# Performance work log

Measured on AMD Instinct MI355X. Metric: run time of the kernel, lower is better.

The kernel has to match this reference:

```python
import jax, jax.numpy as jnp
import numpy as np

IN_DIM = 128
D_MODEL = 2 * IN_DIM        # 256, Mamba d_model
D_INNER = 2 * D_MODEL       # 512, expand=2
D_STATE = 16
D_CONV = 4
DT_RANK = (D_MODEL + 15) // 16  # 16
B = 4
C = 1024                    # original channel dim -> Mamba sequence length
EPS = 1e-5


def rmsnorm(x, w):
    return x * jax.lax.rsqrt(jnp.mean(x * x, axis=-1, keepdims=True) + EPS) * w


def conv1x1(x, w, b):
    # x: (B, Cin, L); 1x1 conv == channel matmul
    return jnp.einsum('oi,bil->bol', w, x) + b[None, :, None]


def mamba(u, in_w, conv_w, conv_b, xproj_w, dt_w, dt_b, A_log, Dp, out_w):
    # u: (B, L, D_MODEL) -- faithful mamba_ssm Mamba block (defaults)
    di, K = conv_w.shape
    n = A_log.shape[1]
    r = dt_w.shape[1]
    xz = u @ in_w.T                              # (B,L,2*di)
    xx, z = jnp.split(xz, 2, axis=-1)
    # depthwise causal conv over L
    xt = jnp.pad(jnp.transpose(xx, (0, 2, 1)), ((0, 0), (0, 0), (K - 1, 0)))
    xc = jax.lax.conv_general_dilated(xt, conv_w[:, None, :], (1,), 'VALID',
                                      feature_group_count=di)
    xx = jax.nn.silu(jnp.transpose(xc + conv_b[None, :, None], (0, 2, 1)))
    dbl = xx @ xproj_w.T                         # (B,L,r+2n)
    dt, Bm, Cm = dbl[..., :r], dbl[..., r:r + n], dbl[..., r + n:]
    dt = jax.nn.softplus(dt @ dt_w.T + dt_b)     # (B,L,di)
    A = -jnp.exp(A_log)                          # (di,n)
    dA = jnp.exp(dt[..., None] * A)              # (B,L,di,n)
    dBx = (dt * xx)[..., None] * Bm[:, :, None, :]

    def step(h, inps):
        dA_t, dBx_t, C_t = inps
        h = dA_t * h + dBx_t
        return h, jnp.einsum('bdn,bn->bd', h, C_t)

    h0 = jnp.zeros((u.shape[0], di, n), u.dtype)
    _, ys = jax.lax.scan(step, h0, (jnp.moveaxis(dA, 1, 0),
                                    jnp.moveaxis(dBx, 1, 0),
                                    jnp.moveaxis(Cm, 1, 0)))
    y = jnp.moveaxis(ys, 0, 1) + xx * Dp
    return (y * jax.nn.silu(z)) @ out_w.T


def postnorm_mamba(u, params, norm_w):
    return rmsnorm(mamba(u, *params), norm_w) + u


def _forward(x, W_in, b_in, W_wp, b_wp, W_fp, b_fp, W_bp, b_bp, W_out, b_out,
             norm_w_top,
             f_in_w, f_conv_w, f_conv_b, f_xproj_w, f_dt_w, f_dt_b, f_A_log, f_D, f_out_w, f_norm_w,
             bk_in_w, bk_conv_w, bk_conv_b, bk_xproj_w, bk_dt_w, bk_dt_b, bk_A_log, bk_D, bk_out_w, bk_norm_w):
    residual = x                                  # (B, C, L)
    xn = rmsnorm(x, norm_w_top)                   # RMSNorm over L
    xt = jnp.transpose(xn, (0, 2, 1))             # (B, L, C); L acts as conv channels
    ssm_in = conv1x1(xt, W_in, b_in)              # (B, 2L, C)
    # forward branch
    fwd = conv1x1(ssm_in, W_fp, b_fp)
    fwd = jnp.transpose(fwd, (0, 2, 1))           # (B, C, 2L): Mamba seq=C
    fwd = postnorm_mamba(fwd, (f_in_w, f_conv_w, f_conv_b, f_xproj_w, f_dt_w,
                               f_dt_b, f_A_log, f_D, f_out_w), f_norm_w)
    fwd = jnp.transpose(fwd, (0, 2, 1))           # (B, 2L, C)
    # backward branch (flip along C)
    bwd = conv1x1(ssm_in[:, :, ::-1], W_bp, b_bp)
    bwd = jnp.transpose(bwd, (0, 2, 1))
    bwd = postnorm_mamba(bwd, (bk_in_w, bk_conv_w, bk_conv_b, bk_xproj_w, bk_dt_w,
                               bk_dt_b, bk_A_log, bk_D, bk_out_w), bk_norm_w)
    bwd = jnp.transpose(bwd, (0, 2, 1))[:, :, ::-1]
    # swish gate
    w = conv1x1(xt, W_wp, b_wp)
    w = w * jax.nn.sigmoid(w)
    out = conv1x1(w * fwd + w * bwd, W_out, b_out)  # (B, L, C)
    return jnp.transpose(out, (0, 2, 1)) + residual  # (B, C, L)


def setup_inputs():
    key = jax.random.key(0)
    ks = iter(jax.random.split(key, 64))
    rn = lambda shape, s=0.02: jax.random.normal(next(ks), shape, jnp.float32) * s
    inp = {"x": jax.random.normal(next(ks), (B, C, IN_DIM), jnp.float32)}
    inp["W_in"] = rn((2 * IN_DIM, IN_DIM));   inp["b_in"] = rn((2 * IN_DIM,), 0.1)
    inp["W_wp"] = rn((2 * IN_DIM, IN_DIM));   inp["b_wp"] = rn((2 * IN_DIM,), 0.1)
    inp["W_fp"] = rn((2 * IN_DIM, 2 * IN_DIM)); inp["b_fp"] = rn((2 * IN_DIM,), 0.1)
    inp["W_bp"] = rn((2 * IN_DIM, 2 * IN_DIM)); inp["b_bp"] = rn((2 * IN_DIM,), 0.1)
    inp["W_out"] = rn((IN_DIM, 2 * IN_DIM));  inp["b_out"] = rn((IN_DIM,), 0.1)
    inp["norm_w_top"] = jnp.ones((IN_DIM,), jnp.float32)
    A_init = jnp.log(jnp.broadcast_to(jnp.arange(1, D_STATE + 1, dtype=jnp.float32),
                                      (D_INNER, D_STATE)))
    for p in ("f", "bk"):
        inp[p + "_in_w"] = rn((2 * D_INNER, D_MODEL))
        inp[p + "_conv_w"] = rn((D_INNER, D_CONV), 0.2)
        inp[p + "_conv_b"] = rn((D_INNER,), 0.1)
        inp[p + "_xproj_w"] = rn((DT_RANK + 2 * D_STATE, D_INNER))
        inp[p + "_dt_w"] = rn((D_INNER, DT_RANK), 0.1)
        inp[p + "_dt_b"] = rn((D_INNER,), 0.5)
        inp[p + "_A_log"] = A_init
        inp[p + "_D"] = jnp.ones((D_INNER,), jnp.float32)
        inp[p + "_out_w"] = rn((D_MODEL, D_INNER))
        inp[p + "_norm_w"] = jnp.ones((D_MODEL,), jnp.float32)
    return inp


def reference(x, W_in, b_in, W_wp, b_wp, W_fp, b_fp, W_bp, b_bp, W_out, b_out,
              norm_w_top,
              f_in_w, f_conv_w, f_conv_b, f_xproj_w, f_dt_w, f_dt_b, f_A_log, f_D, f_out_w, f_norm_w,
              bk_in_w, bk_conv_w, bk_conv_b, bk_xproj_w, bk_dt_w, bk_dt_b, bk_A_log, bk_D, bk_out_w, bk_norm_w):
    return _forward(x, W_in, b_in, W_wp, b_wp, W_fp, b_fp, W_bp, b_bp, W_out, b_out,
                    norm_w_top,
                    f_in_w, f_conv_w, f_conv_b, f_xproj_w, f_dt_w, f_dt_b, f_A_log, f_D, f_out_w, f_norm_w,
                    bk_in_w, bk_conv_w, bk_conv_b, bk_xproj_w, bk_dt_w, bk_dt_b, bk_A_log, bk_D, bk_out_w, bk_norm_w)
```

## Files before the change

kernel.cpp:

```cpp
#include <hip/hip_runtime.h>
#include <math.h>

#define C_LEN 1024
#define NROW 4096
#define NCHUNK 32
#define CHUNK 32

typedef __attribute__((ext_vector_type(8))) short short8;
typedef __attribute__((ext_vector_type(4))) float f32x4;

__device__ __forceinline__ float siluf(float x) { return x / (1.f + __expf(-x)); }

__device__ __forceinline__ unsigned short f2bf(float f) {
    unsigned u = __builtin_bit_cast(unsigned, f);
    unsigned r = (u + 0x7FFFu + ((u >> 16) & 1u)) >> 16;
    return (unsigned short)r;
}
__device__ __forceinline__ float bf2f(unsigned short v) {
    unsigned u = ((unsigned)v) << 16;
    return __builtin_bit_cast(float, u);
}

struct WTab {
    const float* s[11];
    unsigned short* d[11];
    int n[11];
};
__global__ __launch_bounds__(256) void k_prep(WTab t, const float* __restrict__ x,
                                              const float* __restrict__ nw,
                                              unsigned short* __restrict__ xn_bf) {
    int seg = blockIdx.y;
    if (seg < 11) {
        int n = t.n[seg];
        int i = (blockIdx.x * 256 + threadIdx.x) * 4;
        if (i < n) {
            float4 v = *(const float4*)(t.s[seg] + i);
            unsigned short* o = t.d[seg] + i;
            o[0] = f2bf(v.x); o[1] = f2bf(v.y); o[2] = f2bf(v.z); o[3] = f2bf(v.w);
        }
    } else {
        int wave = threadIdx.x >> 6, lane = threadIdx.x & 63;
        #pragma unroll
        for (int it = 0; it < 4; ++it) {
            int row = blockIdx.x * 16 + it * 4 + wave;
            float2 v = ((const float2*)(x + (size_t)row * 128))[lane];
            float ss = v.x * v.x + v.y * v.y;
            #pragma unroll
            for (int off = 32; off; off >>= 1) ss += __shfl_xor(ss, off, 64);
            float rs = rsqrtf(ss * (1.f / 128.f) + 1e-5f);
            float2 wv = ((const float2*)nw)[lane];
            ushort2 o;
            o.x = f2bf(v.x * rs * wv.x);
            o.y = f2bf(v.y * rs * wv.y);
            ((ushort2*)(xn_bf + (size_t)row * 128))[lane] = o;
        }
    }
}

__global__ __launch_bounds__(256) void k_gemm_bf(const unsigned short* __restrict__ A,
                                                 const unsigned short* __restrict__ W,
                                                 const float* __restrict__ bias,
                                                 unsigned short* __restrict__ Cbf,
                                                 int N, int K) {
    __shared__ __align__(16) unsigned short As[64 * 72];
    __shared__ __align__(16) unsigned short Bs[64 * 72];
    int tid = threadIdx.x;
    int m0 = blockIdx.y * 64, n0 = blockIdx.x * 64;
    int w = tid >> 6, lane = tid & 63;
    int q = lane >> 4, ln = lane & 15;
    int srow = tid >> 2;
    int sseg = (tid & 3) * 16;

    const unsigned short* pa = A + (size_t)(m0 + srow) * K + sseg;
    const unsigned short* pw = W + (size_t)(n0 + srow) * K + sseg;

    f32x4 acc[4];
    #pragma unroll
    for (int j = 0; j < 4; ++j) acc[j] = (f32x4)(0.f);

    for (int k0 = 0; k0 < K; k0 += 64) {
        *(short8*)&As[srow * 72 + sseg]     = *(const short8*)pa;
        *(short8*)&As[srow * 72 + sseg + 8] = *(const short8*)(pa + 8);
        *(short8*)&Bs[srow * 72 + sseg]     = *(const short8*)pw;
        *(short8*)&Bs[srow * 72 + sseg + 8] = *(const short8*)(pw + 8);
        pa += 64; pw += 64;
        __syncthreads();
        short8 af0 = *(const short8*)&As[(w * 16 + ln) * 72 + q * 8];
        short8 af1 = *(const short8*)&As[(w * 16 + ln) * 72 + 32 + q * 8];
        #pragma unroll
        for (int j = 0; j < 4; ++j) {
            short8 bf0 = *(const short8*)&Bs[(j * 16 + ln) * 72 + q * 8];
            short8 bf1 = *(const short8*)&Bs[(j * 16 + ln) * 72 + 32 + q * 8];
            acc[j] = __builtin_amdgcn_mfma_f32_16x16x32_bf16(af0, bf0, acc[j], 0, 0, 0);
            acc[j] = __builtin_amdgcn_mfma_f32_16x16x32_bf16(af1, bf1, acc[j], 0, 0, 0);
        }
        __syncthreads();
    }
    #pragma unroll
    for (int j = 0; j < 4; ++j) {
        int nn = n0 + j * 16 + ln;
        float bsv = bias[nn];
        #pragma unroll
        for (int r = 0; r < 4; ++r) {
            int m = m0 + w * 16 + q * 4 + r;
            Cbf[(size_t)m * N + nn] = f2bf(acc[j][r] + bsv);
        }
    }
}

__global__ __launch_bounds__(256) void k_gemm3(
        const unsigned short* __restrict__ xn, const unsigned short* __restrict__ ssm,
        const unsigned short* __restrict__ Wfp, const unsigned short* __restrict__ Wbp,
        const unsigned short* __restrict__ Wwp,
        const float* __restrict__ bfp, const float* __restrict__ bbp,
        const float* __restrict__ bwp,
        unsigned short* __restrict__ uf, unsigned short* __restrict__ ub,
        unsigned short* __restrict__ wbuf) {
    __shared__ __align__(16) unsigned short As[64 * 72];
    __shared__ __align__(16) unsigned short Bs[64 * 72];
    int z = blockIdx.z;
    const unsigned short* A = (z == 2) ? xn : ssm;
    const unsigned short* W = (z == 0) ? Wfp : (z == 1) ? Wbp : Wwp;
    const float* bias = (z == 0) ? bfp : (z == 1) ? bbp : bwp;
    unsigned short* C = (z == 0) ? uf : (z == 1) ? ub : wbuf;
    int K = (z == 2) ? 128 : 256;
    int tid = threadIdx.x;
    int m0 = blockIdx.y * 64, n0 = blockIdx.x * 64;
    int w = tid >> 6, lane = tid & 63;
    int q = lane >> 4, ln = lane & 15;
    int srow = tid >> 2;
    int sseg = (tid & 3) * 16;

    int mLog = m0 + srow;
    int mPhys = (z == 1) ? (mLog ^ (C_LEN - 1)) : mLog;
    const unsigned short* pa = A + (size_t)mPhys * K + sseg;
    const unsigned short* pw = W + (size_t)(n0 + srow) * K + sseg;

    f32x4 acc[4];
    #pragma unroll
    for (int j = 0; j < 4; ++j) acc[j] = (f32x4)(0.f);

    for (int k0 = 0; k0 < K; k0 += 64) {
        *(short8*)&As[srow * 72 + sseg]     = *(const short8*)pa;
        *(short8*)&As[srow * 72 + sseg + 8] = *(const short8*)(pa + 8);
        *(short8*)&Bs[srow * 72 + sseg]     = *(const short8*)pw;
        *(short8*)&Bs[srow * 72 + sseg + 8] = *(const short8*)(pw + 8);
        pa += 64; pw += 64;
        __syncthreads();
        short8 af0 = *(const short8*)&As[(w * 16 + ln) * 72 + q * 8];
        short8 af1 = *(const short8*)&As[(w * 16 + ln) * 72 + 32 + q * 8];
        #pragma unroll
        for (int j = 0; j < 4; ++j) {
            short8 bf0 = *(const short8*)&Bs[(j * 16 + ln) * 72 + q * 8];
            short8 bf1 = *(const short8*)&Bs[(j * 16 + ln) * 72 + 32 + q * 8];
            acc[j] = __builtin_amdgcn_mfma_f32_16x16x32_bf16(af0, bf0, acc[j], 0, 0, 0);
            acc[j] = __builtin_amdgcn_mfma_f32_16x16x32_bf16(af1, bf1, acc[j], 0, 0, 0);
        }
        __syncthreads();
    }
    #pragma unroll
    for (int j = 0; j < 4; ++j) {
        int nn = n0 + j * 16 + ln;
        float bsv = bias[nn];
        #pragma unroll
        for (int r = 0; r < 4; ++r) {
            int m = m0 + w * 16 + q * 4 + r;
            float v = acc[j][r] + bsv;
            if (z == 2) v = siluf(v);
            C[(size_t)m * 256 + nn] = f2bf(v);
        }
    }
}

__global__ __launch_bounds__(256) void k_gemm128(
        const unsigned short* __restrict__ A0, const unsigned short* __restrict__ A1,
        const unsigned short* __restrict__ W0, const unsigned short* __restrict__ W1,
        unsigned short* __restrict__ Cb0, unsigned short* __restrict__ Cb1,
        int N, int K) {
    __shared__ __align__(16) unsigned short As[128 * 72];
    __shared__ __align__(16) unsigned short Bs[64 * 72];
    int p = blockIdx.z;
    const unsigned short* A = p ? A1 : A0;
    const unsigned short* W = p ? W1 : W0;
    unsigned short* Cbf = p ? Cb1 : Cb0;
    int tid = threadIdx.x;
    int m0 = blockIdx.y * 128, n0 = blockIdx.x * 64;
    int w = tid >> 6, lane = tid & 63;
    int q = lane >> 4, ln = lane & 15;

    int arow0 = tid >> 1;
    int aseg0 = (tid & 1) * 32;
    int brow = tid >> 2, bseg = (tid & 3) * 16;
    const unsigned short* pa = A + (size_t)(m0 + arow0) * K + aseg0;
    const unsigned short* pw = W + (size_t)(n0 + brow) * K + bseg;

    f32x4 acc[2][4];
    #pragma unroll
    for (int i = 0; i < 2; ++i)
        #pragma unroll
        for (int j = 0; j < 4; ++j) acc[i][j] = (f32x4)(0.f);

    for (int k0 = 0; k0 < K; k0 += 64) {
        #pragma unroll
        for (int h = 0; h < 4; ++h)
            *(short8*)&As[arow0 * 72 + aseg0 + h * 8] = *(const short8*)(pa + h * 8);
        *(short8*)&Bs[brow * 72 + bseg]     = *(const short8*)pw;
        *(short8*)&Bs[brow * 72 + bseg + 8] = *(const short8*)(pw + 8);
        pa += 64; pw += 64;
        __syncthreads();
        short8 a0[2], a1[2];
        #pragma unroll
        for (int i = 0; i < 2; ++i) {
            int row = w * 32 + i * 16 + ln;
            a0[i] = *(const short8*)&As[row * 72 + q * 8];
            a1[i] = *(const short8*)&As[row * 72 + 32 + q * 8];
        }
        #pragma unroll
        for (int j = 0; j < 4; ++j) {
            short8 bf0 = *(const short8*)&Bs[(j * 16 + ln) * 72 + q * 8];
            short8 bf1 = *(const short8*)&Bs[(j * 16 + ln) * 72 + 32 + q * 8];
            #pragma unroll
            for (int i = 0; i < 2; ++i) {
                acc[i][j] = __builtin_amdgcn_mfma_f32_16x16x32_bf16(a0[i], bf0, acc[i][j], 0, 0, 0);
                acc[i][j] = __builtin_amdgcn_mfma_f32_16x16x32_bf16(a1[i], bf1, acc[i][j], 0, 0, 0);
            }
        }
        __syncthreads();
    }
    #pragma unroll
    for (int i = 0; i < 2; ++i)
        #pragma unroll
        for (int j = 0; j < 4; ++j) {
            int nn = n0 + j * 16 + ln;
            #pragma unroll
            for (int r = 0; r < 4; ++r) {
                int m = m0 + w * 32 + i * 16 + q * 4 + r;
                Cbf[(size_t)m * N + nn] = f2bf(acc[i][j][r]);
            }
        }
}

__global__ __launch_bounds__(256) void k_gemm2f(
        const unsigned short* __restrict__ A0, const unsigned short* __restrict__ A1,
        const unsigned short* __restrict__ W0, const unsigned short* __restrict__ W1,
        float* __restrict__ Cf0, float* __restrict__ Cf1,
        int N, int K) {
    __shared__ __align__(16) unsigned short As[64 * 72];
    __shared__ __align__(16) unsigned short Bs[64 * 72];
    int p = blockIdx.z;
    const unsigned short* A = p ? A1 : A0;
    const unsigned short* W = p ? W1 : W0;
    float* Cf = p ? Cf1 : Cf0;
    int tid = threadIdx.x;
    int m0 = blockIdx.y * 64, n0 = blockIdx.x * 64;
    int w = tid >> 6, lane = tid & 63;
    int q = lane >> 4, ln = lane & 15;
    int srow = tid >> 2;
    int sseg = (tid & 3) * 16;

    const unsigned short* pa = A + (size_t)(m0 + srow) * K + sseg;
    int nIdx = n0 + srow;
    const unsigned short* pw = W + (size_t)nIdx * K + sseg;
    bool nOK = (nIdx < N);

    f32x4 acc[4];
    #pragma unroll
    for (int j = 0; j < 4; ++j) acc[j] = (f32x4)(0.f);

    for (int k0 = 0; k0 < K; k0 += 64) {
        *(short8*)&As[srow * 72 + sseg]     = *(const short8*)pa;
        *(short8*)&As[srow * 72 + sseg + 8] = *(const short8*)(pa + 8);
        short8 b0 = (short8)(0), b1 = (short8)(0);
        if (nOK) { b0 = *(const short8*)pw; b1 = *(const short8*)(pw + 8); }
        *(short8*)&Bs[srow * 72 + sseg] = b0;
        *(short8*)&Bs[srow * 72 + sseg + 8] = b1;
        pa += 64; pw += 64;
        __syncthreads();
        short8 af0 = *(const short8*)&As[(w * 16 + ln) * 72 + q * 8];
        short8 af1 = *(const short8*)&As[(w * 16 + ln) * 72 + 32 + q * 8];
        #pragma unroll
        for (int j = 0; j < 4; ++j) {
            short8 bf0 = *(const short8*)&Bs[(j * 16 + ln) * 72 + q * 8];
            short8 bf1 = *(const short8*)&Bs[(j * 16 + ln) * 72 + 32 + q * 8];
            acc[j] = __builtin_amdgcn_mfma_f32_16x16x32_bf16(af0, bf0, acc[j], 0, 0, 0);
            acc[j] = __builtin_amdgcn_mfma_f32_16x16x32_bf16(af1, bf1, acc[j], 0, 0, 0);
        }
        __syncthreads();
    }
    #pragma unroll
    for (int j = 0; j < 4; ++j) {
        int nn = n0 + j * 16 + ln;
        if (nn < N) {
            #pragma unroll
            for (int r = 0; r < 4; ++r) {
                int m = m0 + w * 16 + q * 4 + r;
                Cf[(size_t)m * N + nn] = acc[j][r];
            }
        }
    }
}

__global__ __launch_bounds__(256) void k_gemm_comb(const unsigned short* __restrict__ wbuf,
                                                   const unsigned short* __restrict__ mof,
                                                   const unsigned short* __restrict__ mob,
                                                   const unsigned short* __restrict__ W,
                                                   const float* __restrict__ bias,
                                                   const float* __restrict__ resid,
                                                   float* __restrict__ Cf,
                                                   int N, int K) {
    __shared__ __align__(16) unsigned short As[64 * 72];
    __shared__ __align__(16) unsigned short Bs[64 * 72];
    int tid = threadIdx.x;
    int m0 = blockIdx.y * 64, n0 = blockIdx.x * 64;
    int w = tid >> 6, lane = tid & 63;
    int q = lane >> 4, ln = lane & 15;
    int srow = tid >> 2;
    int sseg = (tid & 3) * 16;

    int mLog = m0 + srow;
    int mFlip = mLog ^ (C_LEN - 1);
    int nIdx = n0 + srow;
    const unsigned short* pw = W + (size_t)nIdx * K + sseg;
    bool nOK = (nIdx < N);

    f32x4 acc[4];
    #pragma unroll
    for (int j = 0; j < 4; ++j) acc[j] = (f32x4)(0.f);

    for (int k0 = 0; k0 < K; k0 += 64) {
        size_t off  = (size_t)mLog * 256 + k0 + sseg;
        size_t offb = (size_t)mFlip * 256 + k0 + sseg;
        #pragma unroll
        for (int h = 0; h < 2; ++h) {
            short8 aw = *(const short8*)(wbuf + off + h * 8);
            short8 af = *(const short8*)(mof + off + h * 8);
            short8 ab = *(const short8*)(mob + offb + h * 8);
            short8 av;
            #pragma unroll
            for (int j = 0; j < 8; ++j)
                av[j] = (short)f2bf(bf2f((unsigned short)aw[j]) *
                                    (bf2f((unsigned short)af[j]) + bf2f((unsigned short)ab[j])));
            *(short8*)&As[srow * 72 + sseg + h * 8] = av;
        }
        short8 b0 = (short8)(0), b1 = (short8)(0);
        if (nOK) { b0 = *(const short8*)pw; b1 = *(const short8*)(pw + 8); }
        *(short8*)&Bs[srow * 72 + sseg] = b0;
        *(short8*)&Bs[srow * 72 + sseg + 8] = b1;
        pw += 64;
        __syncthreads();
        short8 af0 = *(const short8*)&As[(w * 16 + ln) * 72 + q * 8];
        short8 af1 = *(const short8*)&As[(w * 16 + ln) * 72 + 32 + q * 8];
        #pragma unroll
        for (int j = 0; j < 4; ++j) {
            short8 bf0 = *(const short8*)&Bs[(j * 16 + ln) * 72 + q * 8];
            short8 bf1 = *(const short8*)&Bs[(j * 16 + ln) * 72 + 32 + q * 8];
            acc[j] = __builtin_amdgcn_mfma_f32_16x16x32_bf16(af0, bf0, acc[j], 0, 0, 0);
            acc[j] = __builtin_amdgcn_mfma_f32_16x16x32_bf16(af1, bf1, acc[j], 0, 0, 0);
        }
        __syncthreads();
    }
    #pragma unroll
    for (int j = 0; j < 4; ++j) {
        int nn = n0 + j * 16 + ln;
        if (nn < N) {
            float bsv = bias[nn];
            #pragma unroll
            for (int r = 0; r < 4; ++r) {
                int m = m0 + w * 16 + q * 4 + r;
                Cf[(size_t)m * N + nn] = acc[j][r] + bsv + resid[(size_t)m * N + nn];
            }
        }
    }
}

__global__ __launch_bounds__(256) void k_conv(const unsigned short* __restrict__ xz0,
                                              const unsigned short* __restrict__ xz1,
                                              const float* __restrict__ cw0,
                                              const float* __restrict__ cw1,
                                              const float* __restrict__ cb0,
                                              const float* __restrict__ cb1,
                                              unsigned short* __restrict__ xc0,
                                              unsigned short* __restrict__ xc1) {
    int pz = blockIdx.z;
    const unsigned short* xz = pz ? xz1 : xz0;
    const float* cw = pz ? cw1 : cw0;
    const float* cb = pz ? cb1 : cb0;
    unsigned short* xconv_bf = pz ? xc1 : xc0;
    int d = blockIdx.x * 256 + threadIdx.x;
    int by = blockIdx.y;
    int b = by >> 6, c0 = (by & 63) * 16;
    float4 cwv = *(const float4*)(cw + d * 4);
    float bias = cb[d];
    const unsigned short* base = xz + (size_t)(b * C_LEN) * 1024 + d;
    float w0 = 0.f, w1 = 0.f, w2 = 0.f;
    if (c0) {
        w0 = bf2f(base[(size_t)(c0 - 3) * 1024]);
        w1 = bf2f(base[(size_t)(c0 - 2) * 1024]);
        w2 = bf2f(base[(size_t)(c0 - 1) * 1024]);
    }
    unsigned short* out = xconv_bf + (size_t)(b * C_LEN + c0) * 512 + d;
    #pragma unroll
    for (int i = 0; i < 16; ++i) {
        float cur = bf2f(base[(size_t)(c0 + i) * 1024]);
        float acc = bias;
        acc = fmaf(cwv.x, w0, acc);
        acc = fmaf(cwv.y, w1, acc);
        acc = fmaf(cwv.z, w2, acc);
        acc = fmaf(cwv.w, cur, acc);
        out[(size_t)i * 512] = f2bf(siluf(acc));
        w0 = w1; w1 = w2; w2 = cur;
    }
}

__global__ __launch_bounds__(256) void k_dtproj(const float* __restrict__ dbl0,
                                                const float* __restrict__ dbl1,
                                                const float* __restrict__ dtw0,
                                                const float* __restrict__ dtw1,
                                                const float* __restrict__ dtb0,
                                                const float* __restrict__ dtb1,
                                                unsigned short* __restrict__ dt0,
                                                unsigned short* __restrict__ dt1) {
    int pz = blockIdx.z;
    const float* dbl = pz ? dbl1 : dbl0;
    const float* dtw = pz ? dtw1 : dtw0;
    const float* dtb = pz ? dtb1 : dtb0;
    unsigned short* dt = pz ? dt1 : dt0;
    int d = blockIdx.x * 256 + threadIdx.x;
    int r0 = blockIdx.y * 8;
    float4 w0 = *(const float4*)(dtw + d * 16);
    float4 w1 = *(const float4*)(dtw + d * 16 + 4);
    float4 w2 = *(const float4*)(dtw + d * 16 + 8);
    float4 w3 = *(const float4*)(dtw + d * 16 + 12);
    float bias = dtb[d];
    #pragma unroll
    for (int rr = 0; rr < 8; ++rr) {
        int r = r0 + rr;
        const float* row = dbl + (size_t)r * 48;
        float s = bias;
        s = fmaf(row[0], w0.x, s);  s = fmaf(row[1], w0.y, s);
        s = fmaf(row[2], w0.z, s);  s = fmaf(row[3], w0.w, s);
        s = fmaf(row[4], w1.x, s);  s = fmaf(row[5], w1.y, s);
        s = fmaf(row[6], w1.z, s);  s = fmaf(row[7], w1.w, s);
        s = fmaf(row[8], w2.x, s);  s = fmaf(row[9], w2.y, s);
        s = fmaf(row[10], w2.z, s); s = fmaf(row[11], w2.w, s);
        s = fmaf(row[12], w3.x, s); s = fmaf(row[13], w3.y, s);
        s = fmaf(row[14], w3.z, s); s = fmaf(row[15], w3.w, s);
        float sp = fmaxf(s, 0.f) + log1pf(__expf(-fabsf(s)));
        dt[(size_t)r * 512 + d] = f2bf(sp);
    }
}

__global__ __launch_bounds__(256) void k_scan1(const unsigned short* __restrict__ dt0,
                                               const unsigned short* __restrict__ dt1,
                                               const unsigned short* __restrict__ xc0,
                                               const unsigned short* __restrict__ xc1,
                                               const float* __restrict__ dblA,
                                               const float* __restrict__ dblB,
                                               const float* __restrict__ alog0,
                                               const float* __restrict__ alog1,
                                               float* __restrict__ hfin0,
                                               float* __restrict__ hfin1,
                                               float* __restrict__ Pfin0,
                                               float* __restrict__ Pfin1) {
    int z = blockIdx.z;
    int b = z & 3, p = z >> 2;
    const unsigned short* dt = p ? dt1 : dt0;
    const unsigned short* xconv_bf = p ? xc1 : xc0;
    const float* dbl = p ? dblB : dblA;
    const float* A_log = p ? alog1 : alog0;
    float* hfin = p ? hfin1 : hfin0;
    float* Pfin = p ? Pfin1 : Pfin0;
    int tid = threadIdx.x;
    int nh = tid & 1, dl = tid >> 1;
    int k = blockIdx.x, dg = blockIdx.y;
    int d = dg * 128 + dl;
    float4 al0 = *(const float4*)&A_log[d * 16 + nh * 8];
    float4 al1 = *(const float4*)&A_log[d * 16 + nh * 8 + 4];
    float Ac[8] = {-__expf(al0.x), -__expf(al0.y), -__expf(al0.z), -__expf(al0.w),
                   -__expf(al1.x), -__expf(al1.y), -__expf(al1.z), -__expf(al1.w)};
    size_t r0 = (size_t)(b * C_LEN + k * CHUNK);
    const unsigned short* pdt = dt + r0 * 512 + d;
    const unsigned short* pxv = xconv_bf + r0 * 512 + d;
    const float* pB  = dbl + r0 * 48 + 16 + nh * 8;
    float h[8] = {0.f, 0.f, 0.f, 0.f, 0.f, 0.f, 0.f, 0.f};
    float sdt = 0.f;
    #pragma unroll 8
    for (int c = 0; c < CHUNK; ++c) {
        float dtv = bf2f(*pdt);
        float xv  = bf2f(*pxv);
        float4 B0 = *(const float4*)pB;
        float4 B1 = *(const float4*)(pB + 4);
        float dx = dtv * xv;
        float Bv[8] = {B0.x, B0.y, B0.z, B0.w, B1.x, B1.y, B1.z, B1.w};
        #pragma unroll
        for (int j = 0; j < 8; ++j)
            h[j] = fmaf(__expf(dtv * Ac[j]), h[j], dx * Bv[j]);
        sdt += dtv;
        pdt += 512; pxv += 512; pB += 48;
    }
    size_t idx = ((size_t)(b * NCHUNK + k) * 512 + d) * 16 + nh * 8;
    *(float4*)&hfin[idx]     = make_float4(h[0], h[1], h[2], h[3]);
    *(float4*)&hfin[idx + 4] = make_float4(h[4], h[5], h[6], h[7]);
    *(float4*)&Pfin[idx]     = make_float4(__expf(Ac[0] * sdt), __expf(Ac[1] * sdt),
                                           __expf(Ac[2] * sdt), __expf(Ac[3] * sdt));
    *(float4*)&Pfin[idx + 4] = make_float4(__expf(Ac[4] * sdt), __expf(Ac[5] * sdt),
                                           __expf(Ac[6] * sdt), __expf(Ac[7] * sdt));
}

__global__ __launch_bounds__(256) void k_scan3(const unsigned short* __restrict__ dt0,
                                               const unsigned short* __restrict__ dt1,
                                               const unsigned short* __restrict__ xc0,
                                               const unsigned short* __restrict__ xc1,
                                               const float* __restrict__ dblA,
                                               const float* __restrict__ dblB,
                                               const unsigned short* __restrict__ xz0,
                                               const unsigned short* __restrict__ xz1,
                                               const float* __restrict__ alog0,
                                               const float* __restrict__ alog1,
                                               const float* __restrict__ Dp0,
                                               const float* __restrict__ Dp1,
                                               const float* __restrict__ hfin0,
                                               const float* __restrict__ hfin1,
                                               const float* __restrict__ Pfin0,
                                               const float* __restrict__ Pfin1,
                                               unsigned short* __restrict__ g0,
                                               unsigned short* __restrict__ g1) {
    int z = blockIdx.z;
    int b = z & 3, p = z >> 2;
    const unsigned short* dt = p ? dt1 : dt0;
    const unsigned short* xconv_bf = p ? xc1 : xc0;
    const float* dbl = p ? dblB : dblA;
    const unsigned short* xz = p ? xz1 : xz0;
    const float* A_log = p ? alog1 : alog0;
    const float* Dp = p ? Dp1 : Dp0;
    const float* hfin = p ? hfin1 : hfin0;
    const float* Pfin = p ? Pfin1 : Pfin0;
    unsigned short* gated_bf = p ? g1 : g0;
    int tid = threadIdx.x;
    int nh = tid & 1, dl = tid >> 1;
    int k = blockIdx.x, dg = blockIdx.y;
    int d = dg * 128 + dl;
    float4 al0 = *(const float4*)&A_log[d * 16 + nh * 8];
    float4 al1 = *(const float4*)&A_log[d * 16 + nh * 8 + 4];
    float Ac[8] = {-__expf(al0.x), -__expf(al0.y), -__expf(al0.z), -__expf(al0.w),
                   -__expf(al1.x), -__expf(al1.y), -__expf(al1.z), -__expf(al1.w)};
    float Dd = Dp[d];
    float h[8] = {0.f, 0.f, 0.f, 0.f, 0.f, 0.f, 0.f, 0.f};
    size_t cbase = ((size_t)(b * NCHUNK) * 512 + d) * 16 + nh * 8;
    for (int j = 0; j < k; ++j) {
        size_t idx = cbase + (size_t)j * 8192;
        float4 P0 = *(const float4*)&Pfin[idx];
        float4 P1 = *(const float4*)&Pfin[idx + 4];
        float4 H0 = *(const float4*)&hfin[idx];
        float4 H1 = *(const float4*)&hfin[idx + 4];
        float Pv[8] = {P0.x, P0.y, P0.z, P0.w, P1.x, P1.y, P1.z, P1.w};
        float Hv[8] = {H0.x, H0.y, H0.z, H0.w, H1.x, H1.y, H1.z, H1.w};
        #pragma unroll
        for (int s = 0; s < 8; ++s) h[s] = fmaf(Pv[s], h[s], Hv[s]);
    }
    size_t r0 = (size_t)(b * C_LEN + k * CHUNK);
    const unsigned short* pdt = dt + r0 * 512 + d;
    const unsigned short* pxv = xconv_bf + r0 * 512 + d;
    const float* pB  = dbl + r0 * 48 + 16 + nh * 8;
    const float* pC  = dbl + r0 * 48 + 32 + nh * 8;
    const unsigned short* pz = xz + r0 * 1024 + 512 + d;
    unsigned short* pg = gated_bf + r0 * 512 + d;
    #pragma unroll 4
    for (int c = 0; c < CHUNK; ++c) {
        float dtv = bf2f(*pdt);
        float xv  = bf2f(*pxv);
        float4 B0 = *(const float4*)pB;
        float4 B1 = *(const float4*)(pB + 4);
        float4 C0 = *(const float4*)pC;
        float4 C1 = *(const float4*)(pC + 4);
        float dx = dtv * xv;
        float Bv[8] = {B0.x, B0.y, B0.z, B0.w, B1.x, B1.y, B1.z, B1.w};
        float Cv[8] = {C0.x, C0.y, C0.z, C0.w, C1.x, C1.y, C1.z, C1.w};
        float contrib = 0.f;
        #pragma unroll
        for (int j = 0; j < 8; ++j) {
            h[j] = fmaf(__expf(dtv * Ac[j]), h[j], dx * Bv[j]);
            contrib = fmaf(h[j], Cv[j], contrib);
        }
        contrib += __shfl_xor(contrib, 1, 64);
        if (nh == 0) {
            float y = contrib + xv * Dd;
            float zv = bf2f(*pz);
            *pg = f2bf(y * siluf(zv));
        }
        pdt += 512; pxv += 512; pB += 48; pC += 48; pz += 1024; pg += 512;
    }
}

__global__ __launch_bounds__(256) void k_postnorm(const unsigned short* __restrict__ mo0,
                                                  const unsigned short* __restrict__ mo1,
                                                  const float* __restrict__ w0,
                                                  const float* __restrict__ w1,
                                                  const unsigned short* __restrict__ u0,
                                                  const unsigned short* __restrict__ u1,
                                                  unsigned short* __restrict__ o0,
                                                  unsigned short* __restrict__ o1) {
    __shared__ float red[4];
    int p = blockIdx.y;
    const unsigned short* mo = p ? mo1 : mo0;
    const float* w = p ? w1 : w0;
    const unsigned short* u = p ? u1 : u0;
    unsigned short* out = p ? o1 : o0;
    int r = blockIdx.x, tid = threadIdx.x;
    float v = bf2f(mo[(size_t)r * 256 + tid]);
    float ss = v * v;
    #pragma unroll
    for (int off = 32; off; off >>= 1) ss += __shfl_xor(ss, off, 64);
    if ((tid & 63) == 0) red[tid >> 6] = ss;
    __syncthreads();
    float tot = red[0] + red[1] + red[2] + red[3];
    float rs = rsqrtf(tot * (1.f / 256.f) + 1e-5f);
    out[(size_t)r * 256 + tid] = f2bf(v * rs * w[tid] + bf2f(u[(size_t)r * 256 + tid]));
}

extern "C" void kernel_launch(void* const* d_in, const int* in_sizes, int n_in,
                              void* d_out, int out_size, void* d_ws, size_t ws_size,
                              hipStream_t stream) {
    const float* x          = (const float*)d_in[0];
    const float* W_in       = (const float*)d_in[1];
    const float* b_in       = (const float*)d_in[2];
    const float* W_wp       = (const float*)d_in[3];
    const float* b_wp       = (const float*)d_in[4];
    const float* W_fp       = (const float*)d_in[5];
    const float* b_fp       = (const float*)d_in[6];
    const float* W_bp       = (const float*)d_in[7];
    const float* b_bp       = (const float*)d_in[8];
    const float* W_out      = (const float*)d_in[9];
    const float* b_out      = (const float*)d_in[10];
    const float* norm_w_top = (const float*)d_in[11];
    const float* mamba_p[2][10];
    for (int p = 0; p < 2; ++p)
        for (int i = 0; i < 10; ++i)
            mamba_p[p][i] = (const float*)d_in[12 + p * 10 + i];

    float* ws = (float*)d_ws;
    float* dblP[2]  = {ws + 0,       ws + 196608};
    float* hfinP[2] = {ws + 4587520, ws + 5636096};
    float* PfinP[2] = {ws + 6684672, ws + 7733248};
    unsigned short* dtsP[2] = {(unsigned short*)(ws + 393216),
                               (unsigned short*)(ws + 2490368)};

    unsigned short* us = (unsigned short*)(ws + 8781824);
    unsigned short* xn_bf   = us + 0;
    unsigned short* ssm_bf  = us + 524288;
    unsigned short* uf_bf   = us + 1572864;
    unsigned short* ub_bf   = us + 2621440;
    unsigned short* wbuf_bf = us + 3670016;
    unsigned short* xzP[2]  = {us + 4718592,  us + 8912896};
    unsigned short* xcP[2]  = {us + 13107200, us + 15204352};
    unsigned short* gP[2]   = {us + 17301504, us + 19398656};
    unsigned short* moP[2]  = {us + 21495808, us + 22544384};
    unsigned short* mof_bf  = us + 23592960;
    unsigned short* mob_bf  = us + 24641536;
    unsigned short* wb      = us + 25690112;
    unsigned short* wb_W_in  = wb + 0;
    unsigned short* wb_W_wp  = wb + 32768;
    unsigned short* wb_W_fp  = wb + 65536;
    unsigned short* wb_W_bp  = wb + 131072;
    unsigned short* wb_W_out = wb + 196608;
    unsigned short* wb_in[2]  = {wb + 229376, wb + 647168};
    unsigned short* wb_xp[2]  = {wb + 491520, wb + 909312};
    unsigned short* wb_outw[2]= {wb + 516096, wb + 933888};

    WTab t;
    t.s[0] = W_in;            t.d[0] = wb_W_in;   t.n[0] = 32768;
    t.s[1] = W_wp;            t.d[1] = wb_W_wp;   t.n[1] = 32768;
    t.s[2] = W_fp;            t.d[2] = wb_W_fp;   t.n[2] = 65536;
    t.s[3] = W_bp;            t.d[3] = wb_W_bp;   t.n[3] = 65536;
    t.s[4] = W_out;           t.d[4] = wb_W_out;  t.n[4] = 32768;
    t.s[5] = mamba_p[0][0];   t.d[5] = wb_in[0];  t.n[5] = 262144;
    t.s[6] = mamba_p[0][3];   t.d[6] = wb_xp[0];  t.n[6] = 24576;
    t.s[7] = mamba_p[0][8];   t.d[7] = wb_outw[0];t.n[7] = 131072;
    t.s[8] = mamba_p[1][0];   t.d[8] = wb_in[1];  t.n[8] = 262144;
    t.s[9] = mamba_p[1][3];   t.d[9] = wb_xp[1];  t.n[9] = 24576;
    t.s[10]= mamba_p[1][8];   t.d[10]= wb_outw[1];t.n[10]= 131072;
    k_prep<<<dim3(256, 12), 256, 0, stream>>>(t, x, norm_w_top, xn_bf);

    k_gemm_bf<<<dim3(4, 64), 256, 0, stream>>>(xn_bf, wb_W_in, b_in, ssm_bf, 256, 128);
    k_gemm3<<<dim3(4, 64, 3), 256, 0, stream>>>(xn_bf, ssm_bf, wb_W_fp, wb_W_bp, wb_W_wp,
                                                b_fp, b_bp, b_wp, uf_bf, ub_bf, wbuf_bf);
    k_gemm128<<<dim3(16, 32, 2), 256, 0, stream>>>(uf_bf, ub_bf, wb_in[0], wb_in[1],
                                                   xzP[0], xzP[1], 1024, 256);
    k_conv<<<dim3(2, 256, 2), 256, 0, stream>>>(xzP[0], xzP[1],
                                                mamba_p[0][1], mamba_p[1][1],
                                                mamba_p[0][2], mamba_p[1][2],
                                                xcP[0], xcP[1]);
    k_gemm2f<<<dim3(1, 64, 2), 256, 0, stream>>>(xcP[0], xcP[1], wb_xp[0], wb_xp[1],
                                                 dblP[0], dblP[1], 48, 512);
    k_dtproj<<<dim3(2, 512, 2), 256, 0, stream>>>(dblP[0], dblP[1],
                                                  mamba_p[0][4], mamba_p[1][4],
                                                  mamba_p[0][5], mamba_p[1][5],
                                                  dtsP[0], dtsP[1]);
    k_scan1<<<dim3(NCHUNK, 4, 8), 256, 0, stream>>>(dtsP[0], dtsP[1], xcP[0], xcP[1],
                                                    dblP[0], dblP[1],
                                                    mamba_p[0][6], mamba_p[1][6],
                                                    hfinP[0], hfinP[1], PfinP[0], PfinP[1]);
    k_scan3<<<dim3(NCHUNK, 4, 8), 256, 0, stream>>>(dtsP[0], dtsP[1], xcP[0], xcP[1],
                                                    dblP[0], dblP[1], xzP[0], xzP[1],
                                                    mamba_p[0][6], mamba_p[1][6],
                                                    mamba_p[0][7], mamba_p[1][7],
                                                    hfinP[0], hfinP[1], PfinP[0], PfinP[1],
                                                    gP[0], gP[1]);
    k_gemm128<<<dim3(4, 32, 2), 256, 0, stream>>>(gP[0], gP[1], wb_outw[0], wb_outw[1],
                                                  moP[0], moP[1], 256, 512);
    k_postnorm<<<dim3(NROW, 2), 256, 0, stream>>>(moP[0], moP[1],
                                                  mamba_p[0][9], mamba_p[1][9],
                                                  uf_bf, ub_bf, mof_bf, mob_bf);
    k_gemm_comb<<<dim3(2, 64), 256, 0, stream>>>(wbuf_bf, mof_bf, mob_bf, wb_W_out, b_out,
                                                 x, (float*)d_out, 128, 256);
}
```

Before: 275.2 us.

## Add dedicated inter-chunk carry scan kernel instead of per-block prefix recompute

Adds a k_scan2 kernel that runs a sequential scan over the 32 chunks once per (batch, state element) and writes the incoming carry state in place into the Pfin buffer. k_scan3 then loads one precomputed carry per thread instead of looping over all previous chunks. This removes the quadratic redundant prefix work and repeated hfin/Pfin reads across chunk blocks. The cost is an extra kernel launch and a serial 32-step pass over global memory.

```diff
diff --git a/kernel.cpp b/kernel.cpp
--- a/kernel.cpp
+++ b/kernel.cpp
@@ -507,6 +507,28 @@
                                            __expf(Ac[6] * sdt), __expf(Ac[7] * sdt));
 }
 
+__global__ __launch_bounds__(256) void k_scan2(const float* __restrict__ hfin0,
+                                               const float* __restrict__ hfin1,
+                                               float* __restrict__ Pfin0,
+                                               float* __restrict__ Pfin1) {
+    int tt = blockIdx.x * 256 + threadIdx.x;
+    int p = tt >> 15;
+    int t = tt & 32767;
+    const float* hfin = p ? hfin1 : hfin0;
+    float* Pfin = p ? Pfin1 : Pfin0;
+    int b = t >> 13;
+    int dn = t & 8191;
+    float carry = 0.f;
+    #pragma unroll
+    for (int k = 0; k < NCHUNK; ++k) {
+        size_t idx = (size_t)(b * NCHUNK + k) * 8192 + dn;
+        float pv = Pfin[idx];
+        float hf = hfin[idx];
+        Pfin[idx] = carry;
+        carry = fmaf(pv, carry, hf);
+    }
+}
+
 __global__ __launch_bounds__(256) void k_scan3(const unsigned short* __restrict__ dt0,
                                                const unsigned short* __restrict__ dt1,
                                                const unsigned short* __restrict__ xc0,
@@ -519,10 +541,8 @@
                                                const float* __restrict__ alog1,
                                                const float* __restrict__ Dp0,
                                                const float* __restrict__ Dp1,
-                                               const float* __restrict__ hfin0,
-                                               const float* __restrict__ hfin1,
-                                               const float* __restrict__ Pfin0,
-                                               const float* __restrict__ Pfin1,
+                                               const float* __restrict__ carry0,
+                                               const float* __restrict__ carry1,
                                                unsigned short* __restrict__ g0,
                                                unsigned short* __restrict__ g1) {
     int z = blockIdx.z;
@@ -533,8 +553,7 @@
     const unsigned short* xz = p ? xz1 : xz0;
     const float* A_log = p ? alog1 : alog0;
     const float* Dp = p ? Dp1 : Dp0;
-    const float* hfin = p ? hfin1 : hfin0;
-    const float* Pfin = p ? Pfin1 : Pfin0;
+    const float* carryArr = p ? carry1 : carry0;
     unsigned short* gated_bf = p ? g1 : g0;
     int tid = threadIdx.x;
     int nh = tid & 1, dl = tid >> 1;
@@ -545,19 +564,10 @@
     float Ac[8] = {-__expf(al0.x), -__expf(al0.y), -__expf(al0.z), -__expf(al0.w),
                    -__expf(al1.x), -__expf(al1.y), -__expf(al1.z), -__expf(al1.w)};
     float Dd = Dp[d];
-    float h[8] = {0.f, 0.f, 0.f, 0.f, 0.f, 0.f, 0.f, 0.f};
-    size_t cbase = ((size_t)(b * NCHUNK) * 512 + d) * 16 + nh * 8;
-    for (int j = 0; j < k; ++j) {
-        size_t idx = cbase + (size_t)j * 8192;
-        float4 P0 = *(const float4*)&Pfin[idx];
-        float4 P1 = *(const float4*)&Pfin[idx + 4];
-        float4 H0 = *(const float4*)&hfin[idx];
-        float4 H1 = *(const float4*)&hfin[idx + 4];
-        float Pv[8] = {P0.x, P0.y, P0.z, P0.w, P1.x, P1.y, P1.z, P1.w};
-        float Hv[8] = {H0.x, H0.y, H0.z, H0.w, H1.x, H1.y, H1.z, H1.w};
-        #pragma unroll
-        for (int s = 0; s < 8; ++s) h[s] = fmaf(Pv[s], h[s], Hv[s]);
-    }
+    size_t idx = ((size_t)(b * NCHUNK + k) * 512 + d) * 16 + nh * 8;
+    float4 h0 = *(const float4*)&carryArr[idx];
+    float4 h1 = *(const float4*)&carryArr[idx + 4];
+    float h[8] = {h0.x, h0.y, h0.z, h0.w, h1.x, h1.y, h1.z, h1.w};
     size_t r0 = (size_t)(b * C_LEN + k * CHUNK);
     const unsigned short* pdt = dt + r0 * 512 + d;
     const unsigned short* pxv = xconv_bf + r0 * 512 + d;
@@ -700,12 +710,12 @@
                                                     dblP[0], dblP[1],
                                                     mamba_p[0][6], mamba_p[1][6],
                                                     hfinP[0], hfinP[1], PfinP[0], PfinP[1]);
+    k_scan2<<<256, 256, 0, stream>>>(hfinP[0], hfinP[1], PfinP[0], PfinP[1]);
     k_scan3<<<dim3(NCHUNK, 4, 8), 256, 0, stream>>>(dtsP[0], dtsP[1], xcP[0], xcP[1],
                                                     dblP[0], dblP[1], xzP[0], xzP[1],
                                                     mamba_p[0][6], mamba_p[1][6],
                                                     mamba_p[0][7], mamba_p[1][7],
-                                                    hfinP[0], hfinP[1], PfinP[0], PfinP[1],
-                                                    gP[0], gP[1]);
+                                                    PfinP[0], PfinP[1], gP[0], gP[1]);
     k_gemm128<<<dim3(4, 32, 2), 256, 0, stream>>>(gP[0], gP[1], wb_outw[0], wb_outw[1],
                                                   moP[0], moP[1], 256, 512);
     k_postnorm<<<dim3(NROW, 2), 256, 0, stream>>>(moP[0], moP[1],
```

Measured after the change: 257.4 us, median of 2. -6.5%, faster.
